# Performance work log

Hardware: AMD Instinct MI355X
Metric: run time of the kernel (lower is better)

## Reference

```python
import jax, jax.numpy as jnp
import numpy as np

D_MODEL = 1024
NUM_HEADS = 16
SEQ_LEN = 2048
BATCH = 2
THETA = 10000.0


def apply_rope(x, positions, theta=THETA):
    # x: [b, h, s, d]; positions: [s] int
    d = x.shape[-1]
    inv_freq = 1.0 / (theta ** (jnp.arange(0, d, 2, dtype=jnp.float32) / d))  # [d/2]
    ang = positions.astype(jnp.float32)[:, None] * inv_freq[None, :]  # [s, d/2]
    cos, sin = jnp.cos(ang), jnp.sin(ang)  # [s, d/2]
    x_even = x[..., 0::2]
    x_odd = x[..., 1::2]
    out_even = x_even * cos - x_odd * sin
    out_odd = x_even * sin + x_odd * cos
    # re-interleave pairs
    out = jnp.stack([out_even, out_odd], axis=-1).reshape(x.shape)
    return out


def setup_inputs() -> dict:
    key = jax.random.key(0)
    ks = jax.random.split(key, 5)
    scale = 1.0 / np.sqrt(D_MODEL)
    return {
        "in_features": jax.random.normal(ks[0], (BATCH, SEQ_LEN, D_MODEL), dtype=jnp.float32),
        "token_positions": jnp.arange(SEQ_LEN, dtype=jnp.int32),
        "q_w": jax.random.normal(ks[1], (D_MODEL, D_MODEL), dtype=jnp.float32) * scale,
        "k_w": jax.random.normal(ks[2], (D_MODEL, D_MODEL), dtype=jnp.float32) * scale,
        "v_w": jax.random.normal(ks[3], (D_MODEL, D_MODEL), dtype=jnp.float32) * scale,
        "o_w": jax.random.normal(ks[4], (D_MODEL, D_MODEL), dtype=jnp.float32) * scale,
    }


def reference(in_features, token_positions, q_w, k_w, v_w, o_w):
    b, s, _ = in_features.shape
    h = NUM_HEADS
    d_k = D_MODEL // h

    # Linear stores weights [out, in]: y = x @ W^T
    def proj(x, w):
        y = jnp.einsum('bsi,oi->bso', x, w)
        return y.reshape(b, s, h, d_k).transpose(0, 2, 1, 3)  # [b, h, s, d]

    q = apply_rope(proj(in_features, q_w), token_positions)
    k = apply_rope(proj(in_features, k_w), token_positions)
    v = proj(in_features, v_w)

    scores = jnp.einsum('bhqd,bhkd->bhqk', q, k) / jnp.sqrt(jnp.float32(d_k))
    causal = jnp.tril(jnp.ones((s, s), dtype=bool))
    scores = jnp.where(causal, scores, jnp.float32(-1e30))
    attn = jax.nn.softmax(scores, axis=-1)
    out = jnp.einsum('bhqk,bhkd->bhqd', attn, v)  # [b, h, s, d]
    out = out.transpose(0, 2, 1, 3).reshape(b, s, h * d_k)
    return jnp.einsum('bsi,oi->bso', out, o_w)
```

## Files before the change

### kernel.cpp

```cpp
#include <hip/hip_runtime.h>
#include <hip/hip_bf16.h>

typedef unsigned short ushort_t;
typedef unsigned int uint_t;
typedef __attribute__((ext_vector_type(4))) float f32x4;
typedef __attribute__((ext_vector_type(16))) float f32x16;
typedef __attribute__((ext_vector_type(8))) short short8;
typedef __attribute__((ext_vector_type(4))) short short4x;
typedef __attribute__((ext_vector_type(4))) unsigned short u16x4;
typedef __attribute__((ext_vector_type(2))) uint_t u32x2;

typedef const __attribute__((address_space(1))) unsigned char glob_t;
typedef __attribute__((address_space(3))) unsigned char lds_t;

#define S_LEN 2048
#define DM 1024
#define NH 16
#define DH 64
#define NB 2
#define BH (NB*NH)
#define MROWS (NB*S_LEN)

#define SCALE_L2E 0.18033688f

__device__ __forceinline__ float bf2f(ushort_t u) {
    return __uint_as_float(((uint_t)u) << 16);
}
__device__ __forceinline__ ushort_t f2bf(float f) {
    __hip_bfloat16 h = __float2bfloat16(f);
    return *reinterpret_cast<ushort_t*>(&h);
}

__global__ __launch_bounds__(256) void prep_all(
    const float* __restrict__ X,  const float* __restrict__ Wq,
    const float* __restrict__ Wk, const float* __restrict__ Wv,
    const float* __restrict__ Wo, const int* __restrict__ pos,
    ushort_t* __restrict__ Xb,  ushort_t* __restrict__ Wqb,
    ushort_t* __restrict__ Wkb, ushort_t* __restrict__ Wvb,
    ushort_t* __restrict__ Wob, float2* __restrict__ tab)
{
    int bid = blockIdx.x;
    if (bid < 8192) {
        size_t i = (size_t)bid * 256 + threadIdx.x;
        size_t e = i * 4;
        const float* src; ushort_t* dst; size_t off;
        if (e < (size_t)MROWS * DM) { src = X; dst = Xb; off = e; }
        else {
            size_t r = e - (size_t)MROWS * DM;
            int w = (int)(r >> 20); off = r & 1048575;
            src = (w == 0) ? Wq : (w == 1) ? Wk : (w == 2) ? Wv : Wo;
            dst = (w == 0) ? Wqb : (w == 1) ? Wkb : (w == 2) ? Wvb : Wob;
        }
        float4 v = *reinterpret_cast<const float4*>(src + off);
        u16x4 o;
        o[0] = f2bf(v.x); o[1] = f2bf(v.y); o[2] = f2bf(v.z); o[3] = f2bf(v.w);
        *reinterpret_cast<u16x4*>(dst + off) = o;
    } else {
        int i = (bid - 8192) * 256 + threadIdx.x;
        int s = i >> 5, f = i & 31;
        float inv = powf(10000.0f, -(float)f / 32.0f);
        float ang = (float)pos[s] * inv;
        tab[i] = make_float2(cosf(ang), sinf(ang));
    }
}

template<int MODE>
__global__ __launch_bounds__(256) void gemm128b(
    const ushort_t* __restrict__ A,
    const ushort_t* __restrict__ W0, const ushort_t* __restrict__ W1,
    const ushort_t* __restrict__ W2,
    ushort_t* __restrict__ D0, ushort_t* __restrict__ D1,
    ushort_t* __restrict__ D2,
    float* __restrict__ Fout, const float2* __restrict__ tab)
{
    __shared__ __attribute__((aligned(16))) ushort_t As[128 * 32];
    __shared__ __attribute__((aligned(16))) ushort_t Bs[128 * 32];
    const ushort_t* W = (MODE == 1 || blockIdx.z == 0) ? W0
                        : (blockIdx.z == 1 ? W1 : W2);
    ushort_t* Dst = (blockIdx.z == 0) ? D0 : (blockIdx.z == 1) ? D1 : D2;
    int m0 = blockIdx.x * 128, n0 = blockIdx.y * 128;
    int tid = threadIdx.x, lane = tid & 63, wv = tid >> 6;
    int wm = wv >> 1, wn = wv & 1;
    int l15 = lane & 15, g = lane >> 4;

    f32x4 acc[4][4];
    for (int i = 0; i < 4; i++)
        for (int j = 0; j < 4; j++)
            acc[i][j] = (f32x4){0.f, 0.f, 0.f, 0.f};

    int srow = wv * 32 + (lane >> 2);
    int scol = (lane & 3) * 8;
    const ushort_t* Ap = A + (size_t)(m0 + srow) * DM + scol;
    const ushort_t* Wp = W + (size_t)(n0 + srow) * DM + scol;
    lds_t* laA0 = (lds_t*)&As[wv * 1024];
    lds_t* laA1 = (lds_t*)&As[wv * 1024 + 512];
    lds_t* laB0 = (lds_t*)&Bs[wv * 1024];
    lds_t* laB1 = (lds_t*)&Bs[wv * 1024 + 512];

    for (int kk = 0; kk < DM; kk += 32) {
        __builtin_amdgcn_global_load_lds((glob_t*)(Ap + kk), laA0, 16, 0, 0);
        __builtin_amdgcn_global_load_lds((glob_t*)(Ap + 16 * DM + kk), laA1, 16, 0, 0);
        __builtin_amdgcn_global_load_lds((glob_t*)(Wp + kk), laB0, 16, 0, 0);
        __builtin_amdgcn_global_load_lds((glob_t*)(Wp + 16 * DM + kk), laB1, 16, 0, 0);
        __syncthreads();
        short8 af[4], bf[4];
        for (int i = 0; i < 4; i++)
            af[i] = *reinterpret_cast<const short8*>(
                &As[(wm * 64 + i * 16 + l15) * 32 + g * 8]);
        for (int j = 0; j < 4; j++)
            bf[j] = *reinterpret_cast<const short8*>(
                &Bs[(wn * 64 + j * 16 + l15) * 32 + g * 8]);
        __builtin_amdgcn_s_setprio(1);
        for (int i = 0; i < 4; i++)
            for (int j = 0; j < 4; j++)
                acc[i][j] = __builtin_amdgcn_mfma_f32_16x16x32_bf16(
                    af[i], bf[j], acc[i][j], 0, 0, 0);
        __builtin_amdgcn_s_setprio(0);
        __syncthreads();
    }

    for (int i = 0; i < 4; i++) {
        for (int j = 0; j < 4; j++) {
            int mbase = m0 + wm * 64 + i * 16 + g * 4;
            int n = n0 + wn * 64 + j * 16 + l15;
            if (MODE == 0) {
                int h = n >> 6, d = n & 63;
                if (blockIdx.z < 2) {
                    int f = d >> 1;
                    float sgn = (d & 1) ? 1.f : -1.f;
                    float sc = (blockIdx.z == 0) ? SCALE_L2E : 1.0f;
                    for (int r = 0; r < 4; r++) {
                        int m = mbase + r;
                        int b = m >> 11, s = m & 2047;
                        float v = acc[i][j][r];
                        float p = __shfl_xor(v, 1);
                        float2 cs = tab[s * 32 + f];
                        float out = (v * cs.x + p * cs.y * sgn) * sc;
                        Dst[(((size_t)(b * NH + h)) * S_LEN + s) * DH + d] =
                            f2bf(out);
                    }
                } else {
                    for (int r = 0; r < 4; r++) {
                        int m = mbase + r;
                        int b = m >> 11, s = m & 2047;
                        Dst[((size_t)(b * NH + h) * DH + d) * S_LEN + s] =
                            f2bf(acc[i][j][r]);
                    }
                }
            } else {
                for (int r = 0; r < 4; r++)
                    Fout[(size_t)(mbase + r) * DM + n] = acc[i][j][r];
            }
        }
    }
}

#define WAITV0 asm volatile("s_waitcnt vmcnt(0)" ::: "memory")

__global__ __launch_bounds__(512, 1) void attn_k12(
    const ushort_t* __restrict__ Q, const ushort_t* __restrict__ K,
    const ushort_t* __restrict__ Vt, ushort_t* __restrict__ O)
{
    __shared__ __attribute__((aligned(16))) ushort_t Ks[2][2][8192];
    __shared__ __attribute__((aligned(16))) ushort_t Vs[2][2][8192];

    int tid = threadIdx.x, wv = tid >> 6, lane = tid & 63;
    int l31 = lane & 31, h = lane >> 5, r7 = l31 & 7;
    int bid = blockIdx.x;
    int p = bid >> 5;
    int bh = bid & 31;
    int uB = 15 - p;
    int myu = (wv < 4) ? uB : p;
    int qmin = myu * 128 + (wv & 3) * 32, qmax = qmin + 31;
    int ntr = (uB + 2) >> 1;

    const ushort_t* Qp = Q + (size_t)bh * S_LEN * DH;
    const char* Kp = (const char*)(K + (size_t)bh * S_LEN * DH);
    const char* Vp = (const char*)(Vt + (size_t)bh * DH * S_LEN);

    short8 qf[4];
    {
        const ushort_t* qp = Qp + (((size_t)(qmin + l31)) << 6) + h * 8;
        #pragma unroll
        for (int ds = 0; ds < 4; ds++)
            qf[ds] = *reinterpret_cast<const short8*>(qp + ds * 16);
    }

    f32x16 oacc[2];
    oacc[0] = (f32x16){0.f};
    oacc[1] = (f32x16){0.f};
    float m_run = 0.f, l_run = 0.f;

#define STAGE13(buf, hf, kk0) do {                                            \
    _Pragma("unroll") for (int c_ = 0; c_ < 2; ++c_) {                        \
        int Lk_ = c_ * 8192 + tid * 16;                                       \
        int rk_ = Lk_ >> 7;                                                   \
        int ck_ = (Lk_ & 127) ^ ((rk_ & 7) << 4);                             \
        __builtin_amdgcn_global_load_lds(                                     \
            (glob_t*)(Kp + (size_t)((kk0) + rk_) * 128 + ck_),                \
            (lds_t*)((char*)&Ks[buf][hf][0] + c_ * 8192 + wv * 1024),         \
            16, 0, 0);                                                        \
        int rv_ = Lk_ >> 8;                                                   \
        int cb_ = Lk_ & 255;                                                  \
        int cv_ = ((cb_ & 127) ^ ((rv_ & 7) << 4)) | (cb_ & 128);             \
        __builtin_amdgcn_global_load_lds(                                     \
            (glob_t*)(Vp + (size_t)rv_ * (S_LEN * 2) + (size_t)(kk0) * 2      \
                      + cv_),                                                 \
            (lds_t*)((char*)&Vs[buf][hf][0] + c_ * 8192 + wv * 1024),         \
            16, 0, 0);                                                        \
    } } while (0)

    STAGE13(0, 0, 0);
    STAGE13(0, 1, 128);
    WAITV0;
    __builtin_amdgcn_s_barrier();

    int buf = 0;
    for (int t = 0; t < ntr; ++t) {
        if (t + 1 < ntr) {
            STAGE13(buf ^ 1, 0, (t + 1) * 256);
            STAGE13(buf ^ 1, 1, (t + 1) * 256 + 128);
        }

        #pragma unroll
        for (int hf = 0; hf < 2; ++hf) {
            int k0 = t * 256 + hf * 128;
            if (k0 <= qmax) {
                const char* kb = (const char*)&Ks[buf][hf][0];
                const char* vbp = (const char*)&Vs[buf][hf][0];

                f32x16 st[4];
                #pragma unroll
                for (int s = 0; s < 4; s++) {
                    short8 kf[4];
                    #pragma unroll
                    for (int ds = 0; ds < 4; ds++)
                        kf[ds] = *reinterpret_cast<const short8*>(
                            kb + (s * 32 + l31) * 128
                            + (((h + 2 * ds) ^ r7) << 4));
                    __builtin_amdgcn_s_setprio(1);
                    f32x16 z = {0.f};
                    #pragma unroll
                    for (int ds = 0; ds < 4; ds++)
                        z = __builtin_amdgcn_mfma_f32_32x32x16_bf16(
                            kf[ds], qf[ds], z, 0, 0, 0);
                    st[s] = z;
                    __builtin_amdgcn_s_setprio(0);
                }

                if (k0 + 127 > qmin) {
                    int q = qmin + l31;
                    #pragma unroll
                    for (int s = 0; s < 4; s++)
                        #pragma unroll
                        for (int r = 0; r < 16; r++)
                            if ((k0 + s * 32 + (r & 3) + 8 * (r >> 2) + 4 * h) > q)
                                st[s][r] = -1e30f;
                }

                if (t == 0 && hf == 0) {
                    float mv[4];
                    #pragma unroll
                    for (int s = 0; s < 4; s++) {
                        float a0 = fmaxf(st[s][0], st[s][1]);
                        float a1 = fmaxf(st[s][2], st[s][3]);
                        float a2 = fmaxf(st[s][4], st[s][5]);
                        float a3 = fmaxf(st[s][6], st[s][7]);
                        float a4 = fmaxf(st[s][8], st[s][9]);
                        float a5 = fmaxf(st[s][10], st[s][11]);
                        float a6 = fmaxf(st[s][12], st[s][13]);
                        float a7 = fmaxf(st[s][14], st[s][15]);
                        mv[s] = fmaxf(fmaxf(fmaxf(a0, a1), fmaxf(a2, a3)),
                                      fmaxf(fmaxf(a4, a5), fmaxf(a6, a7)));
                    }
                    float m16 = fmaxf(fmaxf(mv[0], mv[1]),
                                      fmaxf(mv[2], mv[3]));
                    m16 = fmaxf(m16, __shfl_xor(m16, 32));
                    m_run = m16 + 8.0f;
                }

                float ps = 0.f;
                short4x pa[4][4];
                #pragma unroll
                for (int s = 0; s < 4; s++)
                    #pragma unroll
                    for (int kt = 0; kt < 4; kt++) {
                        float p0 = exp2f(st[s][4 * kt + 0] - m_run);
                        float p1 = exp2f(st[s][4 * kt + 1] - m_run);
                        float p2 = exp2f(st[s][4 * kt + 2] - m_run);
                        float p3 = exp2f(st[s][4 * kt + 3] - m_run);
                        ps += (p0 + p1) + (p2 + p3);
                        u32x2 w = { (uint_t)f2bf(p0) | ((uint_t)f2bf(p1) << 16),
                                    (uint_t)f2bf(p2) | ((uint_t)f2bf(p3) << 16) };
                        pa[s][kt] = __builtin_bit_cast(short4x, w);
                    }
                l_run += ps;

                #pragma unroll
                for (int s = 0; s < 4; s++) {
                    short4x vb[2][4];
                    #pragma unroll
                    for (int db = 0; db < 2; db++)
                        #pragma unroll
                        for (int kt = 0; kt < 4; kt++) {
                            int c = s * 4 + kt;
                            vb[db][kt] = *reinterpret_cast<const short4x*>(
                                vbp + (db * 32 + l31) * 256
                                + ((((c & 7) ^ r7) << 4) | ((c >> 3) << 7))
                                + h * 8);
                        }
                    __builtin_amdgcn_s_setprio(1);
                    #pragma unroll
                    for (int kt = 0; kt < 4; kt++) {
                        oacc[0] = __builtin_amdgcn_mfma_f32_32x32x8bf16_1k(
                            vb[0][kt], pa[s][kt], oacc[0], 0, 0, 0);
                        oacc[1] = __builtin_amdgcn_mfma_f32_32x32x8bf16_1k(
                            vb[1][kt], pa[s][kt], oacc[1], 0, 0, 0);
                    }
                    __builtin_amdgcn_s_setprio(0);
                }
            }
        }

        WAITV0;
        __builtin_amdgcn_s_barrier();
        buf ^= 1;
    }

    l_run += __shfl_xor(l_run, 32);
    float inv = 1.0f / l_run;
    int b = bh >> 4, head = bh & 15;
    int q_row = qmin + l31;
    size_t obase = ((size_t)b * S_LEN + q_row) * DM + head * DH;
    #pragma unroll
    for (int db = 0; db < 2; db++)
        #pragma unroll
        for (int rg = 0; rg < 4; rg++) {
            u16x4 o;
            #pragma unroll
            for (int j = 0; j < 4; j++)
                o[j] = f2bf(oacc[db][rg * 4 + j] * inv);
            *reinterpret_cast<u16x4*>(&O[obase + db * 32 + rg * 8 + h * 4]) = o;
        }
#undef STAGE13
}

extern "C" void kernel_launch(void* const* d_in, const int* in_sizes, int n_in,
                              void* d_out, int out_size, void* d_ws, size_t ws_size,
                              hipStream_t stream)
{
    const float* X  = (const float*)d_in[0];
    const int* pos  = (const int*)d_in[1];
    const float* qw = (const float*)d_in[2];
    const float* kw = (const float*)d_in[3];
    const float* vw = (const float*)d_in[4];
    const float* ow = (const float*)d_in[5];
    float* out = (float*)d_out;

    char* ws = (char*)d_ws;
    ushort_t* Xb   = (ushort_t*)(ws);
    ushort_t* Wqb  = (ushort_t*)(ws + 8388608);
    ushort_t* Wkb  = (ushort_t*)(ws + 10485760);
    ushort_t* Wvb  = (ushort_t*)(ws + 12582912);
    ushort_t* Wob  = (ushort_t*)(ws + 14680064);
    ushort_t* Qbh  = (ushort_t*)(ws + 16777216);
    ushort_t* Kbh  = (ushort_t*)(ws + 25165824);
    ushort_t* Vtb  = (ushort_t*)(ws + 41943040);
    ushort_t* AttO = (ushort_t*)(ws + 50331648);
    float2*   tab  = (float2*)(ws + 58720256);

    prep_all<<<8448, 256, 0, stream>>>(X, qw, kw, vw, ow, pos,
                                       Xb, Wqb, Wkb, Wvb, Wob, tab);
    gemm128b<0><<<dim3(32, 8, 3), 256, 0, stream>>>(
        Xb, Wqb, Wkb, Wvb, Qbh, Kbh, Vtb, nullptr, tab);
    attn_k12<<<256, 512, 0, stream>>>(Qbh, Kbh, Vtb, AttO);
    gemm128b<1><<<dim3(32, 8, 1), 256, 0, stream>>>(
        AttO, Wob, nullptr, nullptr, nullptr, nullptr, nullptr, out, tab);
}
```

Measured before the change: 123.9 us.

## Split attention KV range across wave halves and merge partial softmax in LDS

Each block now handles a single 128-query tile. The two groups of four waves process alternating 128-key halves of each 256-key chunk, and their partial outputs, sums and maxima are merged through LDS at the end. The grid doubles to 512 blocks, LDS shrinks to a single buffer, and launch bounds allow up to 4 blocks per CU, raising occupancy. The cost is the loss of double-buffered prefetch: loads are now issued between two barriers, which serialises transfer and compute inside a block. It also adds a merge step at the end.

```diff
diff --git a/kernel.cpp b/kernel.cpp
--- a/kernel.cpp
+++ b/kernel.cpp
@@ -157,22 +157,21 @@
 
 #define WAITV0 asm volatile("s_waitcnt vmcnt(0)" ::: "memory")
 
-__global__ __launch_bounds__(512, 1) void attn_k12(
+__global__ __launch_bounds__(512, 4) void attn_k13(
     const ushort_t* __restrict__ Q, const ushort_t* __restrict__ K,
     const ushort_t* __restrict__ Vt, ushort_t* __restrict__ O)
 {
-    __shared__ __attribute__((aligned(16))) ushort_t Ks[2][2][8192];
-    __shared__ __attribute__((aligned(16))) ushort_t Vs[2][2][8192];
+    __shared__ __attribute__((aligned(16))) ushort_t Ks[2][8192];
+    __shared__ __attribute__((aligned(16))) ushort_t Vs[2][8192];
 
     int tid = threadIdx.x, wv = tid >> 6, lane = tid & 63;
     int l31 = lane & 31, h = lane >> 5, r7 = l31 & 7;
     int bid = blockIdx.x;
-    int p = bid >> 5;
+    int u = (bid < 256) ? (15 - (bid >> 5)) : ((bid - 256) >> 5);
     int bh = bid & 31;
-    int uB = 15 - p;
-    int myu = (wv < 4) ? uB : p;
-    int qmin = myu * 128 + (wv & 3) * 32, qmax = qmin + 31;
-    int ntr = (uB + 2) >> 1;
+    int qsub = wv & 3, hf = wv >> 2;
+    int qmin = u * 128 + qsub * 32, qmax = qmin + 31;
+    int ntr = (u + 2) >> 1;
 
     const ushort_t* Qp = Q + (size_t)bh * S_LEN * DH;
     const char* Kp = (const char*)(K + (size_t)bh * S_LEN * DH);
@@ -189,16 +188,16 @@
     f32x16 oacc[2];
     oacc[0] = (f32x16){0.f};
     oacc[1] = (f32x16){0.f};
-    float m_run = 0.f, l_run = 0.f;
-
-#define STAGE13(buf, hf, kk0) do {                                            \
+    float m_run = -1e20f, l_run = 0.f;
+
+#define STAGE14(hfs, kk0) do {                                                \
     _Pragma("unroll") for (int c_ = 0; c_ < 2; ++c_) {                        \
         int Lk_ = c_ * 8192 + tid * 16;                                       \
         int rk_ = Lk_ >> 7;                                                   \
         int ck_ = (Lk_ & 127) ^ ((rk_ & 7) << 4);                             \
         __builtin_amdgcn_global_load_lds(                                     \
             (glob_t*)(Kp + (size_t)((kk0) + rk_) * 128 + ck_),                \
-            (lds_t*)((char*)&Ks[buf][hf][0] + c_ * 8192 + wv * 1024),         \
+            (lds_t*)((char*)&Ks[hfs][0] + c_ * 8192 + wv * 1024),             \
             16, 0, 0);                                                        \
         int rv_ = Lk_ >> 8;                                                   \
         int cb_ = Lk_ & 255;                                                  \
@@ -206,143 +205,162 @@
         __builtin_amdgcn_global_load_lds(                                     \
             (glob_t*)(Vp + (size_t)rv_ * (S_LEN * 2) + (size_t)(kk0) * 2      \
                       + cv_),                                                 \
-            (lds_t*)((char*)&Vs[buf][hf][0] + c_ * 8192 + wv * 1024),         \
+            (lds_t*)((char*)&Vs[hfs][0] + c_ * 8192 + wv * 1024),             \
             16, 0, 0);                                                        \
     } } while (0)
 
-    STAGE13(0, 0, 0);
-    STAGE13(0, 1, 128);
+    STAGE14(0, 0);
+    STAGE14(1, 128);
     WAITV0;
     __builtin_amdgcn_s_barrier();
 
-    int buf = 0;
     for (int t = 0; t < ntr; ++t) {
-        if (t + 1 < ntr) {
-            STAGE13(buf ^ 1, 0, (t + 1) * 256);
-            STAGE13(buf ^ 1, 1, (t + 1) * 256 + 128);
-        }
-
-        #pragma unroll
-        for (int hf = 0; hf < 2; ++hf) {
-            int k0 = t * 256 + hf * 128;
-            if (k0 <= qmax) {
-                const char* kb = (const char*)&Ks[buf][hf][0];
-                const char* vbp = (const char*)&Vs[buf][hf][0];
-
-                f32x16 st[4];
-                #pragma unroll
-                for (int s = 0; s < 4; s++) {
-                    short8 kf[4];
-                    #pragma unroll
-                    for (int ds = 0; ds < 4; ds++)
-                        kf[ds] = *reinterpret_cast<const short8*>(
-                            kb + (s * 32 + l31) * 128
-                            + (((h + 2 * ds) ^ r7) << 4));
-                    __builtin_amdgcn_s_setprio(1);
-                    f32x16 z = {0.f};
-                    #pragma unroll
-                    for (int ds = 0; ds < 4; ds++)
-                        z = __builtin_amdgcn_mfma_f32_32x32x16_bf16(
-                            kf[ds], qf[ds], z, 0, 0, 0);
-                    st[s] = z;
-                    __builtin_amdgcn_s_setprio(0);
-                }
-
-                if (k0 + 127 > qmin) {
-                    int q = qmin + l31;
-                    #pragma unroll
-                    for (int s = 0; s < 4; s++)
-                        #pragma unroll
-                        for (int r = 0; r < 16; r++)
-                            if ((k0 + s * 32 + (r & 3) + 8 * (r >> 2) + 4 * h) > q)
-                                st[s][r] = -1e30f;
-                }
-
-                if (t == 0 && hf == 0) {
-                    float mv[4];
-                    #pragma unroll
-                    for (int s = 0; s < 4; s++) {
-                        float a0 = fmaxf(st[s][0], st[s][1]);
-                        float a1 = fmaxf(st[s][2], st[s][3]);
-                        float a2 = fmaxf(st[s][4], st[s][5]);
-                        float a3 = fmaxf(st[s][6], st[s][7]);
-                        float a4 = fmaxf(st[s][8], st[s][9]);
-                        float a5 = fmaxf(st[s][10], st[s][11]);
-                        float a6 = fmaxf(st[s][12], st[s][13]);
-                        float a7 = fmaxf(st[s][14], st[s][15]);
-                        mv[s] = fmaxf(fmaxf(fmaxf(a0, a1), fmaxf(a2, a3)),
-                                      fmaxf(fmaxf(a4, a5), fmaxf(a6, a7)));
-                    }
-                    float m16 = fmaxf(fmaxf(mv[0], mv[1]),
-                                      fmaxf(mv[2], mv[3]));
-                    m16 = fmaxf(m16, __shfl_xor(m16, 32));
-                    m_run = m16 + 8.0f;
-                }
-
-                float ps = 0.f;
-                short4x pa[4][4];
+        int k0 = t * 256 + hf * 128;
+        if (k0 <= qmax) {
+            const char* kb = (const char*)&Ks[hf][0];
+            const char* vbp = (const char*)&Vs[hf][0];
+
+            f32x16 st[4];
+            #pragma unroll
+            for (int s = 0; s < 4; s++) {
+                short8 kf[4];
+                #pragma unroll
+                for (int ds = 0; ds < 4; ds++)
+                    kf[ds] = *reinterpret_cast<const short8*>(
+                        kb + (s * 32 + l31) * 128
+                        + (((h + 2 * ds) ^ r7) << 4));
+                __builtin_amdgcn_s_setprio(1);
+                f32x16 z = {0.f};
+                #pragma unroll
+                for (int ds = 0; ds < 4; ds++)
+                    z = __builtin_amdgcn_mfma_f32_32x32x16_bf16(
+                        kf[ds], qf[ds], z, 0, 0, 0);
+                st[s] = z;
+                __builtin_amdgcn_s_setprio(0);
+            }
+
+            if (k0 + 127 > qmin) {
+                int q = qmin + l31;
                 #pragma unroll
                 for (int s = 0; s < 4; s++)
                     #pragma unroll
-                    for (int kt = 0; kt < 4; kt++) {
-                        float p0 = exp2f(st[s][4 * kt + 0] - m_run);
-                        float p1 = exp2f(st[s][4 * kt + 1] - m_run);
-                        float p2 = exp2f(st[s][4 * kt + 2] - m_run);
-                        float p3 = exp2f(st[s][4 * kt + 3] - m_run);
-                        ps += (p0 + p1) + (p2 + p3);
-                        u32x2 w = { (uint_t)f2bf(p0) | ((uint_t)f2bf(p1) << 16),
-                                    (uint_t)f2bf(p2) | ((uint_t)f2bf(p3) << 16) };
-                        pa[s][kt] = __builtin_bit_cast(short4x, w);
-                    }
-                l_run += ps;
-
+                    for (int r = 0; r < 16; r++)
+                        if ((k0 + s * 32 + (r & 3) + 8 * (r >> 2) + 4 * h) > q)
+                            st[s][r] = -1e30f;
+            }
+
+            if (t == 0) {
+                float mv[4];
                 #pragma unroll
                 for (int s = 0; s < 4; s++) {
-                    short4x vb[2][4];
-                    #pragma unroll
-                    for (int db = 0; db < 2; db++)
-                        #pragma unroll
-                        for (int kt = 0; kt < 4; kt++) {
-                            int c = s * 4 + kt;
-                            vb[db][kt] = *reinterpret_cast<const short4x*>(
-                                vbp + (db * 32 + l31) * 256
-                                + ((((c & 7) ^ r7) << 4) | ((c >> 3) << 7))
-                                + h * 8);
-                        }
-                    __builtin_amdgcn_s_setprio(1);
+                    float a0 = fmaxf(st[s][0], st[s][1]);
+                    float a1 = fmaxf(st[s][2], st[s][3]);
+                    float a2 = fmaxf(st[s][4], st[s][5]);
+                    float a3 = fmaxf(st[s][6], st[s][7]);
+                    float a4 = fmaxf(st[s][8], st[s][9]);
+                    float a5 = fmaxf(st[s][10], st[s][11]);
+                    float a6 = fmaxf(st[s][12], st[s][13]);
+                    float a7 = fmaxf(st[s][14], st[s][15]);
+                    mv[s] = fmaxf(fmaxf(fmaxf(a0, a1), fmaxf(a2, a3)),
+                                  fmaxf(fmaxf(a4, a5), fmaxf(a6, a7)));
+                }
+                float m16 = fmaxf(fmaxf(mv[0], mv[1]), fmaxf(mv[2], mv[3]));
+                m16 = fmaxf(m16, __shfl_xor(m16, 32));
+                m_run = m16 + 8.0f;
+            }
+
+            float ps = 0.f;
+            short4x pa[4][4];
+            #pragma unroll
+            for (int s = 0; s < 4; s++)
+                #pragma unroll
+                for (int kt = 0; kt < 4; kt++) {
+                    float p0 = exp2f(st[s][4 * kt + 0] - m_run);
+                    float p1 = exp2f(st[s][4 * kt + 1] - m_run);
+                    float p2 = exp2f(st[s][4 * kt + 2] - m_run);
+                    float p3 = exp2f(st[s][4 * kt + 3] - m_run);
+                    ps += (p0 + p1) + (p2 + p3);
+                    u32x2 w = { (uint_t)f2bf(p0) | ((uint_t)f2bf(p1) << 16),
+                                (uint_t)f2bf(p2) | ((uint_t)f2bf(p3) << 16) };
+                    pa[s][kt] = __builtin_bit_cast(short4x, w);
+                }
+            l_run += ps;
+
+            #pragma unroll
+            for (int s = 0; s < 4; s++) {
+                short4x vb[2][4];
+                #pragma unroll
+                for (int db = 0; db < 2; db++)
                     #pragma unroll
                     for (int kt = 0; kt < 4; kt++) {
-                        oacc[0] = __builtin_amdgcn_mfma_f32_32x32x8bf16_1k(
-                            vb[0][kt], pa[s][kt], oacc[0], 0, 0, 0);
-                        oacc[1] = __builtin_amdgcn_mfma_f32_32x32x8bf16_1k(
-                            vb[1][kt], pa[s][kt], oacc[1], 0, 0, 0);
+                        int c = s * 4 + kt;
+                        vb[db][kt] = *reinterpret_cast<const short4x*>(
+                            vbp + (db * 32 + l31) * 256
+                            + ((((c & 7) ^ r7) << 4) | ((c >> 3) << 7))
+                            + h * 8);
                     }
-                    __builtin_amdgcn_s_setprio(0);
-                }
-            }
-        }
-
-        WAITV0;
+                __builtin_amdgcn_s_setprio(1);
+                #pragma unroll
+                for (int kt = 0; kt < 4; kt++) {
+                    oacc[0] = __builtin_amdgcn_mfma_f32_32x32x8bf16_1k(
+                        vb[0][kt], pa[s][kt], oacc[0], 0, 0, 0);
+                    oacc[1] = __builtin_amdgcn_mfma_f32_32x32x8bf16_1k(
+                        vb[1][kt], pa[s][kt], oacc[1], 0, 0, 0);
+                }
+                __builtin_amdgcn_s_setprio(0);
+            }
+        }
+
         __builtin_amdgcn_s_barrier();
-        buf ^= 1;
-    }
-
-    l_run += __shfl_xor(l_run, 32);
-    float inv = 1.0f / l_run;
-    int b = bh >> 4, head = bh & 15;
-    int q_row = qmin + l31;
-    size_t obase = ((size_t)b * S_LEN + q_row) * DM + head * DH;
-    #pragma unroll
-    for (int db = 0; db < 2; db++)
-        #pragma unroll
-        for (int rg = 0; rg < 4; rg++) {
-            u16x4 o;
-            #pragma unroll
-            for (int j = 0; j < 4; j++)
-                o[j] = f2bf(oacc[db][rg * 4 + j] * inv);
-            *reinterpret_cast<u16x4*>(&O[obase + db * 32 + rg * 8 + h * 4]) = o;
-        }
-#undef STAGE13
+        if (t + 1 < ntr) {
+            STAGE14(0, (t + 1) * 256);
+            STAGE14(1, (t + 1) * 256 + 128);
+            WAITV0;
+        }
+        __builtin_amdgcn_s_barrier();
+    }
+
+    {
+        float* smK = (float*)&Ks[0][0];
+        float* smV = (float*)&Vs[0][0];
+        float* base = (qsub < 2) ? smK : smV;
+        float* slot = base + ((qsub & 1) * 64 + lane) * 34;
+        if (hf == 1) {
+            #pragma unroll
+            for (int j = 0; j < 16; j++) slot[j] = oacc[0][j];
+            #pragma unroll
+            for (int j = 0; j < 16; j++) slot[16 + j] = oacc[1][j];
+            slot[32] = l_run;
+            slot[33] = m_run;
+        }
+        __syncthreads();
+        if (hf == 0) {
+            float lB = slot[32], mB = slot[33];
+            float ms = fmaxf(m_run, mB);
+            float fa = exp2f(m_run - ms), fb = exp2f(mB - ms);
+            float l_tot = l_run * fa + lB * fb;
+            l_tot += __shfl_xor(l_tot, 32);
+            float inv = 1.0f / l_tot;
+            int b = bh >> 4, head = bh & 15;
+            int q_row = qmin + l31;
+            size_t obase = ((size_t)b * S_LEN + q_row) * DM + head * DH;
+            #pragma unroll
+            for (int db = 0; db < 2; db++)
+                #pragma unroll
+                for (int rg = 0; rg < 4; rg++) {
+                    u16x4 o;
+                    #pragma unroll
+                    for (int j = 0; j < 4; j++) {
+                        float v = oacc[db][rg * 4 + j] * fa
+                                + slot[db * 16 + rg * 4 + j] * fb;
+                        o[j] = f2bf(v * inv);
+                    }
+                    *reinterpret_cast<u16x4*>(
+                        &O[obase + db * 32 + rg * 8 + h * 4]) = o;
+                }
+        }
+    }
+#undef STAGE14
 }
 
 extern "C" void kernel_launch(void* const* d_in, const int* in_sizes, int n_in,
@@ -373,7 +391,7 @@
                                        Xb, Wqb, Wkb, Wvb, Wob, tab);
     gemm128b<0><<<dim3(32, 8, 3), 256, 0, stream>>>(
         Xb, Wqb, Wkb, Wvb, Qbh, Kbh, Vtb, nullptr, tab);
-    attn_k12<<<256, 512, 0, stream>>>(Qbh, Kbh, Vtb, AttO);
+    attn_k13<<<512, 512, 0, stream>>>(Qbh, Kbh, Vtb, AttO);
     gemm128b<1><<<dim3(32, 8, 1), 256, 0, stream>>>(
         AttO, Wob, nullptr, nullptr, nullptr, nullptr, nullptr, out, tab);
 }
```

After: 168.2 us. 35.7% more time.

## Split attention into one-tile blocks with single-buffered K/V staging

Applied to the files above, without the earlier changes.

The attention kernel moves from 256 blocks of 512 threads, where each block paired a long and a short causal query tile, to 512 blocks of 256 threads that each handle one 128-query tile. The K/V staging drops the double-buffered 256-key prefetch and uses a single 128-key LDS buffer that is loaded after each step's compute, with barriers around the load. The intent is to cut per-block LDS and thread count so several blocks can share a CU and hide latency through occupancy instead of explicit prefetching. The cost is that loads no longer overlap compute inside a block, and causal load balance now relies on the hardware scheduler rather than the tile pairing.

```diff
diff --git a/kernel.cpp b/kernel.cpp
--- a/kernel.cpp
+++ b/kernel.cpp
@@ -157,22 +157,19 @@
 
 #define WAITV0 asm volatile("s_waitcnt vmcnt(0)" ::: "memory")
 
-__global__ __launch_bounds__(512, 1) void attn_k12(
+__global__ __launch_bounds__(256) void attn_k14(
     const ushort_t* __restrict__ Q, const ushort_t* __restrict__ K,
     const ushort_t* __restrict__ Vt, ushort_t* __restrict__ O)
 {
-    __shared__ __attribute__((aligned(16))) ushort_t Ks[2][2][8192];
-    __shared__ __attribute__((aligned(16))) ushort_t Vs[2][2][8192];
+    __shared__ __attribute__((aligned(16))) ushort_t Ks[8192];
+    __shared__ __attribute__((aligned(16))) ushort_t Vs[8192];
 
     int tid = threadIdx.x, wv = tid >> 6, lane = tid & 63;
     int l31 = lane & 31, h = lane >> 5, r7 = l31 & 7;
     int bid = blockIdx.x;
-    int p = bid >> 5;
+    int u = 15 - (bid >> 5);
     int bh = bid & 31;
-    int uB = 15 - p;
-    int myu = (wv < 4) ? uB : p;
-    int qmin = myu * 128 + (wv & 3) * 32, qmax = qmin + 31;
-    int ntr = (uB + 2) >> 1;
+    int qmin = u * 128 + wv * 32;
 
     const ushort_t* Qp = Q + (size_t)bh * S_LEN * DH;
     const char* Kp = (const char*)(K + (size_t)bh * S_LEN * DH);
@@ -191,140 +188,127 @@
     oacc[1] = (f32x16){0.f};
     float m_run = 0.f, l_run = 0.f;
 
-#define STAGE13(buf, hf, kk0) do {                                            \
-    _Pragma("unroll") for (int c_ = 0; c_ < 2; ++c_) {                        \
-        int Lk_ = c_ * 8192 + tid * 16;                                       \
-        int rk_ = Lk_ >> 7;                                                   \
-        int ck_ = (Lk_ & 127) ^ ((rk_ & 7) << 4);                             \
+#define STAGE15(kk0) do {                                                     \
+    _Pragma("unroll") for (int c_ = 0; c_ < 4; ++c_) {                        \
+        int L_ = c_ * 4096 + tid * 16;                                        \
+        int rk_ = L_ >> 7;                                                    \
+        int ck_ = (L_ & 127) ^ ((rk_ & 7) << 4);                              \
         __builtin_amdgcn_global_load_lds(                                     \
             (glob_t*)(Kp + (size_t)((kk0) + rk_) * 128 + ck_),                \
-            (lds_t*)((char*)&Ks[buf][hf][0] + c_ * 8192 + wv * 1024),         \
-            16, 0, 0);                                                        \
-        int rv_ = Lk_ >> 8;                                                   \
-        int cb_ = Lk_ & 255;                                                  \
+            (lds_t*)((char*)&Ks[0] + c_ * 4096 + wv * 1024), 16, 0, 0);       \
+        int rv_ = L_ >> 8;                                                    \
+        int cb_ = L_ & 255;                                                   \
         int cv_ = ((cb_ & 127) ^ ((rv_ & 7) << 4)) | (cb_ & 128);             \
         __builtin_amdgcn_global_load_lds(                                     \
             (glob_t*)(Vp + (size_t)rv_ * (S_LEN * 2) + (size_t)(kk0) * 2      \
                       + cv_),                                                 \
-            (lds_t*)((char*)&Vs[buf][hf][0] + c_ * 8192 + wv * 1024),         \
-            16, 0, 0);                                                        \
+            (lds_t*)((char*)&Vs[0] + c_ * 4096 + wv * 1024), 16, 0, 0);       \
     } } while (0)
 
-    STAGE13(0, 0, 0);
-    STAGE13(0, 1, 128);
+    STAGE15(0);
     WAITV0;
     __builtin_amdgcn_s_barrier();
 
-    int buf = 0;
-    for (int t = 0; t < ntr; ++t) {
-        if (t + 1 < ntr) {
-            STAGE13(buf ^ 1, 0, (t + 1) * 256);
-            STAGE13(buf ^ 1, 1, (t + 1) * 256 + 128);
-        }
-
-        #pragma unroll
-        for (int hf = 0; hf < 2; ++hf) {
-            int k0 = t * 256 + hf * 128;
-            if (k0 <= qmax) {
-                const char* kb = (const char*)&Ks[buf][hf][0];
-                const char* vbp = (const char*)&Vs[buf][hf][0];
-
-                f32x16 st[4];
+    for (int t = 0; t <= u; ++t) {
+        int k0 = t << 7;
+        const char* kb = (const char*)&Ks[0];
+        const char* vbp = (const char*)&Vs[0];
+
+        f32x16 st[4];
+        #pragma unroll
+        for (int s = 0; s < 4; s++) {
+            short8 kf[4];
+            #pragma unroll
+            for (int ds = 0; ds < 4; ds++)
+                kf[ds] = *reinterpret_cast<const short8*>(
+                    kb + (s * 32 + l31) * 128 + (((h + 2 * ds) ^ r7) << 4));
+            __builtin_amdgcn_s_setprio(1);
+            f32x16 z = {0.f};
+            #pragma unroll
+            for (int ds = 0; ds < 4; ds++)
+                z = __builtin_amdgcn_mfma_f32_32x32x16_bf16(
+                    kf[ds], qf[ds], z, 0, 0, 0);
+            st[s] = z;
+            __builtin_amdgcn_s_setprio(0);
+        }
+
+        if (t == u) {
+            int q = qmin + l31;
+            #pragma unroll
+            for (int s = 0; s < 4; s++)
                 #pragma unroll
-                for (int s = 0; s < 4; s++) {
-                    short8 kf[4];
-                    #pragma unroll
-                    for (int ds = 0; ds < 4; ds++)
-                        kf[ds] = *reinterpret_cast<const short8*>(
-                            kb + (s * 32 + l31) * 128
-                            + (((h + 2 * ds) ^ r7) << 4));
-                    __builtin_amdgcn_s_setprio(1);
-                    f32x16 z = {0.f};
-                    #pragma unroll
-                    for (int ds = 0; ds < 4; ds++)
-                        z = __builtin_amdgcn_mfma_f32_32x32x16_bf16(
-                            kf[ds], qf[ds], z, 0, 0, 0);
-                    st[s] = z;
-                    __builtin_amdgcn_s_setprio(0);
+                for (int r = 0; r < 16; r++)
+                    if ((k0 + s * 32 + (r & 3) + 8 * (r >> 2) + 4 * h) > q)
+                        st[s][r] = -1e30f;
+        }
+
+        if (t == 0) {
+            float mv[4];
+            #pragma unroll
+            for (int s = 0; s < 4; s++) {
+                float a0 = fmaxf(st[s][0], st[s][1]);
+                float a1 = fmaxf(st[s][2], st[s][3]);
+                float a2 = fmaxf(st[s][4], st[s][5]);
+                float a3 = fmaxf(st[s][6], st[s][7]);
+                float a4 = fmaxf(st[s][8], st[s][9]);
+                float a5 = fmaxf(st[s][10], st[s][11]);
+                float a6 = fmaxf(st[s][12], st[s][13]);
+                float a7 = fmaxf(st[s][14], st[s][15]);
+                mv[s] = fmaxf(fmaxf(fmaxf(a0, a1), fmaxf(a2, a3)),
+                              fmaxf(fmaxf(a4, a5), fmaxf(a6, a7)));
+            }
+            float m16 = fmaxf(fmaxf(mv[0], mv[1]), fmaxf(mv[2], mv[3]));
+            m16 = fmaxf(m16, __shfl_xor(m16, 32));
+            m_run = m16 + 8.0f;
+        }
+
+        float ps = 0.f;
+        short4x pa[4][4];
+        #pragma unroll
+        for (int s = 0; s < 4; s++)
+            #pragma unroll
+            for (int kt = 0; kt < 4; kt++) {
+                float p0 = exp2f(st[s][4 * kt + 0] - m_run);
+                float p1 = exp2f(st[s][4 * kt + 1] - m_run);
+                float p2 = exp2f(st[s][4 * kt + 2] - m_run);
+                float p3 = exp2f(st[s][4 * kt + 3] - m_run);
+                ps += (p0 + p1) + (p2 + p3);
+                u32x2 w = { (uint_t)f2bf(p0) | ((uint_t)f2bf(p1) << 16),
+                            (uint_t)f2bf(p2) | ((uint_t)f2bf(p3) << 16) };
+                pa[s][kt] = __builtin_bit_cast(short4x, w);
+            }
+        l_run += ps;
+
+        #pragma unroll
+        for (int s = 0; s < 4; s++) {
+            short4x vb[2][4];
+            #pragma unroll
+            for (int db = 0; db < 2; db++)
+                #pragma unroll
+                for (int kt = 0; kt < 4; kt++) {
+                    int c = s * 4 + kt;
+                    vb[db][kt] = *reinterpret_cast<const short4x*>(
+                        vbp + (db * 32 + l31) * 256
+                        + ((((c & 7) ^ r7) << 4) | ((c >> 3) << 7))
+                        + h * 8);
                 }
-
-                if (k0 + 127 > qmin) {
-                    int q = qmin + l31;
-                    #pragma unroll
-                    for (int s = 0; s < 4; s++)
-                        #pragma unroll
-                        for (int r = 0; r < 16; r++)
-                            if ((k0 + s * 32 + (r & 3) + 8 * (r >> 2) + 4 * h) > q)
-                                st[s][r] = -1e30f;
-                }
-
-                if (t == 0 && hf == 0) {
-                    float mv[4];
-                    #pragma unroll
-                    for (int s = 0; s < 4; s++) {
-                        float a0 = fmaxf(st[s][0], st[s][1]);
-                        float a1 = fmaxf(st[s][2], st[s][3]);
-                        float a2 = fmaxf(st[s][4], st[s][5]);
-                        float a3 = fmaxf(st[s][6], st[s][7]);
-                        float a4 = fmaxf(st[s][8], st[s][9]);
-                        float a5 = fmaxf(st[s][10], st[s][11]);
-                        float a6 = fmaxf(st[s][12], st[s][13]);
-                        float a7 = fmaxf(st[s][14], st[s][15]);
-                        mv[s] = fmaxf(fmaxf(fmaxf(a0, a1), fmaxf(a2, a3)),
-                                      fmaxf(fmaxf(a4, a5), fmaxf(a6, a7)));
-                    }
-                    float m16 = fmaxf(fmaxf(mv[0], mv[1]),
-                                      fmaxf(mv[2], mv[3]));
-                    m16 = fmaxf(m16, __shfl_xor(m16, 32));
-                    m_run = m16 + 8.0f;
-                }
-
-                float ps = 0.f;
-                short4x pa[4][4];
-                #pragma unroll
-                for (int s = 0; s < 4; s++)
-                    #pragma unroll
-                    for (int kt = 0; kt < 4; kt++) {
-                        float p0 = exp2f(st[s][4 * kt + 0] - m_run);
-                        float p1 = exp2f(st[s][4 * kt + 1] - m_run);
-                        float p2 = exp2f(st[s][4 * kt + 2] - m_run);
-                        float p3 = exp2f(st[s][4 * kt + 3] - m_run);
-                        ps += (p0 + p1) + (p2 + p3);
-                        u32x2 w = { (uint_t)f2bf(p0) | ((uint_t)f2bf(p1) << 16),
-                                    (uint_t)f2bf(p2) | ((uint_t)f2bf(p3) << 16) };
-                        pa[s][kt] = __builtin_bit_cast(short4x, w);
-                    }
-                l_run += ps;
-
-                #pragma unroll
-                for (int s = 0; s < 4; s++) {
-                    short4x vb[2][4];
-                    #pragma unroll
-                    for (int db = 0; db < 2; db++)
-                        #pragma unroll
-                        for (int kt = 0; kt < 4; kt++) {
-                            int c = s * 4 + kt;
-                            vb[db][kt] = *reinterpret_cast<const short4x*>(
-                                vbp + (db * 32 + l31) * 256
-                                + ((((c & 7) ^ r7) << 4) | ((c >> 3) << 7))
-                                + h * 8);
-                        }
-                    __builtin_amdgcn_s_setprio(1);
-                    #pragma unroll
-                    for (int kt = 0; kt < 4; kt++) {
-                        oacc[0] = __builtin_amdgcn_mfma_f32_32x32x8bf16_1k(
-                            vb[0][kt], pa[s][kt], oacc[0], 0, 0, 0);
-                        oacc[1] = __builtin_amdgcn_mfma_f32_32x32x8bf16_1k(
-                            vb[1][kt], pa[s][kt], oacc[1], 0, 0, 0);
-                    }
-                    __builtin_amdgcn_s_setprio(0);
-                }
+            __builtin_amdgcn_s_setprio(1);
+            #pragma unroll
+            for (int kt = 0; kt < 4; kt++) {
+                oacc[0] = __builtin_amdgcn_mfma_f32_32x32x8bf16_1k(
+                    vb[0][kt], pa[s][kt], oacc[0], 0, 0, 0);
+                oacc[1] = __builtin_amdgcn_mfma_f32_32x32x8bf16_1k(
+                    vb[1][kt], pa[s][kt], oacc[1], 0, 0, 0);
             }
-        }
-
-        WAITV0;
+            __builtin_amdgcn_s_setprio(0);
+        }
+
         __builtin_amdgcn_s_barrier();
-        buf ^= 1;
+        if (t < u) {
+            STAGE15((t + 1) << 7);
+            WAITV0;
+        }
+        __builtin_amdgcn_s_barrier();
     }
 
     l_run += __shfl_xor(l_run, 32);
@@ -342,7 +326,7 @@
                 o[j] = f2bf(oacc[db][rg * 4 + j] * inv);
             *reinterpret_cast<u16x4*>(&O[obase + db * 32 + rg * 8 + h * 4]) = o;
         }
-#undef STAGE13
+#undef STAGE15
 }
 
 extern "C" void kernel_launch(void* const* d_in, const int* in_sizes, int n_in,
@@ -373,7 +357,7 @@
                                        Xb, Wqb, Wkb, Wvb, Wob, tab);
     gemm128b<0><<<dim3(32, 8, 3), 256, 0, stream>>>(
         Xb, Wqb, Wkb, Wvb, Qbh, Kbh, Vtb, nullptr, tab);
-    attn_k12<<<256, 512, 0, stream>>>(Qbh, Kbh, Vtb, AttO);
+    attn_k14<<<512, 256, 0, stream>>>(Qbh, Kbh, Vtb, AttO);
     gemm128b<1><<<dim3(32, 8, 1), 256, 0, stream>>>(
         AttO, Wob, nullptr, nullptr, nullptr, nullptr, nullptr, out, tab);
 }
```

New measurement: 136.4 us. +10.0%, slower.
